# Optimization experiments

Hardware: AMD Instinct MI355X
Metric: run time of the kernel (lower is better)

## Reference

```python
import jax, jax.numpy as jnp
import numpy as np

LEVELS, REGIONS, Z_SIZE = 4, 8, 16
PHI_SIZE, OUT_SIZE, HIDDEN = 64, 32, 64
BATCH = 256
IN_SIZE = LEVELS * Z_SIZE + PHI_SIZE  # 128


def setup_inputs() -> dict:
    key = jax.random.key(0)
    ks = jax.random.split(key, 8)
    return {
        "phi": jax.random.normal(ks[0], (BATCH, PHI_SIZE), dtype=jnp.float32),
        "region_params": jax.random.normal(ks[1], (LEVELS, REGIONS, Z_SIZE), dtype=jnp.float32),
        "w1": jax.random.normal(ks[2], (HIDDEN, IN_SIZE), dtype=jnp.float32) * (1.0 / np.sqrt(IN_SIZE)),
        "b1": jax.random.normal(ks[3], (HIDDEN,), dtype=jnp.float32) * 0.01,
        "w2": jax.random.normal(ks[4], (HIDDEN, HIDDEN), dtype=jnp.float32) * (1.0 / np.sqrt(HIDDEN)),
        "b2": jax.random.normal(ks[5], (HIDDEN,), dtype=jnp.float32) * 0.01,
        "w3": jax.random.normal(ks[6], (OUT_SIZE, HIDDEN), dtype=jnp.float32) * (1.0 / np.sqrt(HIDDEN)),
        "b3": jax.random.normal(ks[7], (OUT_SIZE,), dtype=jnp.float32) * 0.01,
    }


def reference(phi, region_params, w1, b1, w2, b2, w3, b3):
    levels, regions, z_size = region_params.shape
    phi = phi.reshape(phi.shape[0], -1)
    batch, dim = phi.shape
    # Combinatorial grid of region choices per level (same as source: mgrid + .T indexing)
    i = jnp.mgrid[(slice(0, regions, 1),) * levels]  # (levels, regions, ..., regions)
    V_alphas = region_params[jnp.arange(levels), i.T].reshape(-1, levels * z_size)  # (R^L, latent_dim)
    n_combo = V_alphas.shape[0]
    phi_b = jnp.broadcast_to(phi[:, None, :], (batch, n_combo, dim))
    V_b = jnp.broadcast_to(V_alphas[None], (batch, n_combo, levels * z_size))
    X = jnp.concatenate([V_b, phi_b], axis=-1)  # (batch, R^L, in_size)
    # MLP: Linear->relu->Linear->relu->Linear
    h = jax.nn.relu(jnp.einsum("bci,hi->bch", X, w1) + b1)
    h = jax.nn.relu(jnp.einsum("bch,gh->bcg", h, w2) + b2)
    qs = jnp.einsum("bcg,og->bco", h, w3) + b3  # (batch, R^L, out_size)
    return qs
```

## Files before the change

kernel.cpp:

```cpp
#include <hip/hip_runtime.h>
#include <hip/hip_bf16.h>


typedef __attribute__((ext_vector_type(8))) short bf16x8;
typedef __attribute__((ext_vector_type(4))) short bf16x4;
typedef __attribute__((ext_vector_type(4))) float f32x4;

#define MFMA_K32(a, b, c) __builtin_amdgcn_mfma_f32_16x16x32_bf16(a, b, c, 0, 0, 0)

#if defined(__has_builtin)
#if __has_builtin(__builtin_amdgcn_mfma_f32_16x16x16bf16_1k)
#define MFMA_K16(a, b, c) __builtin_amdgcn_mfma_f32_16x16x16bf16_1k(a, b, c, 0, 0, 0)
#elif __has_builtin(__builtin_amdgcn_mfma_f32_16x16x16_bf16)
#define MFMA_K16(a, b, c) __builtin_amdgcn_mfma_f32_16x16x16_bf16(a, b, c, 0, 0, 0)
#endif
#endif
#ifndef MFMA_K16
__device__ __forceinline__ f32x4 mfma_k16_asm(bf16x4 a, bf16x4 b, f32x4 c) {
    f32x4 d;
    asm("v_mfma_f32_16x16x16_bf16 %0, %1, %2, %3" : "=v"(d) : "v"(a), "v"(b), "v"(c));
    return d;
}
#define MFMA_K16(a, b, c) mfma_k16_asm(a, b, c)
#endif

__device__ __forceinline__ short f2bf(float x) {
    union { __hip_bfloat16 b; short s; } u;
    u.b = __float2bfloat16(x);
    return u.s;
}

__device__ __forceinline__ float4 ldg4(const float* p) {
    return *reinterpret_cast<const float4*>(p);
}

__global__ __launch_bounds__(256, 4)
void zdec_kernel(const float* __restrict__ phi, const float* __restrict__ rp,
                 const float* __restrict__ w1, const float* __restrict__ b1,
                 const float* __restrict__ w2, const float* __restrict__ b2,
                 const float* __restrict__ w3, const float* __restrict__ b3,
                 float* __restrict__ out)
{
    __shared__ float smem[8256];
    float* const A01 = smem;
    float* const Bt  = smem + 4096;
    float* const Pt  = smem + 6144;
    float* const Ot  = smem + 6208;

    const int t   = threadIdx.x;
    const int b   = blockIdx.x >> 2;
    const int cbi = blockIdx.x & 3;

    {
        const int l = t >> 6, h = t & 63;
        float ws[16];
#pragma unroll
        for (int z4 = 0; z4 < 4; ++z4) {
            const float4 v = ldg4(w1 + h * 128 + l * 16 + z4 * 4);
            ws[z4*4+0] = v.x; ws[z4*4+1] = v.y; ws[z4*4+2] = v.z; ws[z4*4+3] = v.w;
        }
#pragma unroll
        for (int r = 0; r < 8; ++r) {
            float acc = 0.f;
#pragma unroll
            for (int z4 = 0; z4 < 4; ++z4) {
                const float4 v = ldg4(rp + (l * 8 + r) * 16 + z4 * 4);
                acc += ws[z4*4+0]*v.x + ws[z4*4+1]*v.y + ws[z4*4+2]*v.z + ws[z4*4+3]*v.w;
            }
            Bt[(l * 8 + r) * 64 + h] = acc;
        }
    }
    if (t < 64) {
        const int h = t;
        float acc = b1[h];
#pragma unroll
        for (int p4 = 0; p4 < 16; ++p4) {
            const float4 wv = ldg4(w1 + h * 128 + 64 + p4 * 4);
            const float4 pv = ldg4(phi + b * 64 + p4 * 4);
            acc += wv.x * pv.x + wv.y * pv.y + wv.z * pv.z + wv.w * pv.w;
        }
        Pt[h] = acc;
    }
    __syncthreads();
    {
        const int h = t & 63, cg = t >> 6;
#pragma unroll
        for (int cc2 = 0; cc2 < 16; ++cc2) {
            const int cc = cg * 16 + cc2;
            A01[cc * 64 + (h ^ ((cc & 15) << 2))] =
                Bt[(cc & 7) * 64 + h] + Bt[(8 + ((cc >> 3) & 7)) * 64 + h];
        }
    }
    __syncthreads();

    const int lane = t & 63;
    const int wid  = t >> 6;
    const int q = lane >> 4;
    const int s = lane & 15;
    const int row = (wid << 4) + s;
    const int amask = s << 2;

    bf16x8 w2f[4][2];
#pragma unroll
    for (int nt = 0; nt < 4; ++nt)
#pragma unroll
        for (int kt = 0; kt < 2; ++kt) {
            const float* src = w2 + (nt * 16 + s) * 64 + kt * 32 + q * 8;
            const float4 v0 = ldg4(src), v1 = ldg4(src + 4);
            bf16x8 f;
            f[0]=f2bf(v0.x); f[1]=f2bf(v0.y); f[2]=f2bf(v0.z); f[3]=f2bf(v0.w);
            f[4]=f2bf(v1.x); f[5]=f2bf(v1.y); f[6]=f2bf(v1.z); f[7]=f2bf(v1.w);
            w2f[nt][kt] = f;
        }
    bf16x4 w3f[2][4];
#pragma unroll
    for (int nt3 = 0; nt3 < 2; ++nt3)
#pragma unroll
        for (int nt = 0; nt < 4; ++nt) {
            const float4 v = ldg4(w3 + (nt3 * 16 + s) * 64 + nt * 16 + q * 4);
            bf16x4 f;
            f[0]=f2bf(v.x); f[1]=f2bf(v.y); f[2]=f2bf(v.z); f[3]=f2bf(v.w);
            w3f[nt3][nt] = f;
        }
    f32x4 b2i[4];
#pragma unroll
    for (int nt = 0; nt < 4; ++nt) {
        const float4 v = ldg4(b2 + nt * 16 + q * 4);
        b2i[nt] = f32x4{v.x, v.y, v.z, v.w};
    }
    f32x4 b3i[2];
#pragma unroll
    for (int nt3 = 0; nt3 < 2; ++nt3) {
        const float4 v = ldg4(b3 + nt3 * 16 + q * 4);
        b3i[nt3] = f32x4{v.x, v.y, v.z, v.w};
    }

    float* const ot = Ot + (wid << 9);
    float* const gwbase = out + ((size_t)b * 4096 + (cbi << 10) + (wid << 4)) * 32;

    for (int mhi = 0; mhi < 2; ++mhi) {
        const float* bt3 = Bt + (24 + (((cbi << 1) + mhi) & 7)) * 64;
        float ap3[16];
#pragma unroll
        for (int c4 = 0; c4 < 4; ++c4) {
            const int hc = (c4 >> 1) * 32 + q * 8 + (c4 & 1) * 4;
            const f32x4 av = *reinterpret_cast<const f32x4*>(A01 + row * 64 + (hc ^ amask));
            const f32x4 pv = *reinterpret_cast<const f32x4*>(Pt + hc);
            const f32x4 v3 = *reinterpret_cast<const f32x4*>(bt3 + hc);
#pragma unroll
            for (int j = 0; j < 4; ++j) ap3[c4*4+j] = av[j] + pv[j] + v3[j];
        }
#pragma unroll
        for (int mlo = 0; mlo < 8; ++mlo) {
            const float* bt2 = Bt + (16 + mlo) * 64;
            bf16x8 h1f0, h1f1;
            {
                float tmp[16];
#pragma unroll
                for (int c4 = 0; c4 < 4; ++c4) {
                    const int hc = (c4 >> 1) * 32 + q * 8 + (c4 & 1) * 4;
                    const f32x4 v2 = *reinterpret_cast<const f32x4*>(bt2 + hc);
#pragma unroll
                    for (int j = 0; j < 4; ++j)
                        tmp[c4*4+j] = fmaxf(ap3[c4*4+j] + v2[j], 0.f);
                }
#pragma unroll
                for (int j = 0; j < 8; ++j) h1f0[j] = f2bf(tmp[j]);
#pragma unroll
                for (int j = 0; j < 8; ++j) h1f1[j] = f2bf(tmp[8 + j]);
            }
            f32x4 a2[4];
#pragma unroll
            for (int nt = 0; nt < 4; ++nt) {
                f32x4 acc = b2i[nt];
                acc = MFMA_K32(w2f[nt][0], h1f0, acc);
                acc = MFMA_K32(w2f[nt][1], h1f1, acc);
                a2[nt] = acc;
            }
            bf16x4 h2f[4];
#pragma unroll
            for (int nt = 0; nt < 4; ++nt) {
                bf16x4 f;
#pragma unroll
                for (int r = 0; r < 4; ++r) f[r] = f2bf(fmaxf(a2[nt][r], 0.f));
                h2f[nt] = f;
            }
#pragma unroll
            for (int nt3 = 0; nt3 < 2; ++nt3) {
                f32x4 acc = b3i[nt3];
#pragma unroll
                for (int nt = 0; nt < 4; ++nt)
                    acc = MFMA_K16(w3f[nt3][nt], h2f[nt], acc);
                const int c = (nt3 * 4 + q) ^ (s & 7);
                *reinterpret_cast<f32x4*>(ot + s * 32 + c * 4) = acc;
            }
            asm volatile("s_waitcnt lgkmcnt(0)" ::: "memory");
            {
                float* gb = gwbase + (mhi * 8 + mlo) * 2048;
#pragma unroll
                for (int k = 0; k < 2; ++k) {
                    const int sr = k * 8 + (lane >> 3);
                    const int cr = (lane & 7) ^ (sr & 7);
                    const f32x4 v = *reinterpret_cast<const f32x4*>(ot + sr * 32 + cr * 4);
                    *reinterpret_cast<f32x4*>(gb + k * 256 + lane * 4) = v;
                }
            }
        }
    }
}

extern "C" void kernel_launch(void* const* d_in, const int* in_sizes, int n_in,
                              void* d_out, int out_size, void* d_ws, size_t ws_size,
                              hipStream_t stream) {
    const float* phi = (const float*)d_in[0];
    const float* rp  = (const float*)d_in[1];
    const float* w1  = (const float*)d_in[2];
    const float* b1  = (const float*)d_in[3];
    const float* w2  = (const float*)d_in[4];
    const float* b2  = (const float*)d_in[5];
    const float* w3  = (const float*)d_in[6];
    const float* b3  = (const float*)d_in[7];
    (void)in_sizes; (void)n_in; (void)out_size; (void)d_ws; (void)ws_size;

    zdec_kernel<<<dim3(1024), dim3(256), 0, stream>>>(
        phi, rp, w1, b1, w2, b2, w3, b3, (float*)d_out);
}
```

Measured before the change: 42.28 us.

## Drop A01 LDS staging, keep layer-1 sums in registers, defer output stores

Removes the shared-memory A01 table and its extra barrier. Each thread now builds its two level-0/1/3 plus phi partial sums directly in registers from Bt. The loop order is swapped so the level-2 row is loaded once per mlo. Each tile's global store is deferred until the next tile's compute and the explicit lgkmcnt wait is dropped, so LDS readback and global writes overlap with MFMA work. LDS use roughly halves, which may allow more resident blocks, at the cost of extra registers for the two partial-sum arrays.

```diff
diff --git a/kernel.cpp b/kernel.cpp
--- a/kernel.cpp
+++ b/kernel.cpp
@@ -41,11 +41,10 @@
                  const float* __restrict__ w3, const float* __restrict__ b3,
                  float* __restrict__ out)
 {
-    __shared__ float smem[8256];
-    float* const A01 = smem;
-    float* const Bt  = smem + 4096;
-    float* const Pt  = smem + 6144;
-    float* const Ot  = smem + 6208;
+    __shared__ float smem[4160];
+    float* const Bt = smem;
+    float* const Pt = smem + 2048;
+    float* const Ot = smem + 2112;
 
     const int t   = threadIdx.x;
     const int b   = blockIdx.x >> 2;
@@ -80,16 +79,6 @@
             acc += wv.x * pv.x + wv.y * pv.y + wv.z * pv.z + wv.w * pv.w;
         }
         Pt[h] = acc;
-    }
-    __syncthreads();
-    {
-        const int h = t & 63, cg = t >> 6;
-#pragma unroll
-        for (int cc2 = 0; cc2 < 16; ++cc2) {
-            const int cc = cg * 16 + cc2;
-            A01[cc * 64 + (h ^ ((cc & 15) << 2))] =
-                Bt[(cc & 7) * 64 + h] + Bt[(8 + ((cc >> 3) & 7)) * 64 + h];
-        }
     }
     __syncthreads();
 
@@ -98,7 +87,6 @@
     const int q = lane >> 4;
     const int s = lane & 15;
     const int row = (wid << 4) + s;
-    const int amask = s << 2;
 
     bf16x8 w2f[4][2];
 #pragma unroll
@@ -135,35 +123,65 @@
         b3i[nt3] = f32x4{v.x, v.y, v.z, v.w};
     }
 
+    float afp[2][16];
+    {
+        const float* a0  = Bt + ((row & 7)) * 64;
+        const float* a1  = Bt + (8 + ((row >> 3) & 7)) * 64;
+        const float* t3a = Bt + (24 + 2 * cbi) * 64;
+        const float* t3b = Bt + (24 + 2 * cbi + 1) * 64;
+#pragma unroll
+        for (int c4 = 0; c4 < 4; ++c4) {
+            const int hc = (c4 >> 1) * 32 + q * 8 + (c4 & 1) * 4;
+            const f32x4 v0 = *reinterpret_cast<const f32x4*>(a0 + hc);
+            const f32x4 v1 = *reinterpret_cast<const f32x4*>(a1 + hc);
+            const f32x4 vp = *reinterpret_cast<const f32x4*>(Pt + hc);
+            const f32x4 w0 = *reinterpret_cast<const f32x4*>(t3a + hc);
+            const f32x4 w1v = *reinterpret_cast<const f32x4*>(t3b + hc);
+#pragma unroll
+            for (int j = 0; j < 4; ++j) {
+                const float base = v0[j] + v1[j] + vp[j];
+                afp[0][c4*4+j] = base + w0[j];
+                afp[1][c4*4+j] = base + w1v[j];
+            }
+        }
+    }
+
     float* const ot = Ot + (wid << 9);
     float* const gwbase = out + ((size_t)b * 4096 + (cbi << 10) + (wid << 4)) * 32;
 
-    for (int mhi = 0; mhi < 2; ++mhi) {
-        const float* bt3 = Bt + (24 + (((cbi << 1) + mhi) & 7)) * 64;
-        float ap3[16];
-#pragma unroll
-        for (int c4 = 0; c4 < 4; ++c4) {
-            const int hc = (c4 >> 1) * 32 + q * 8 + (c4 & 1) * 4;
-            const f32x4 av = *reinterpret_cast<const f32x4*>(A01 + row * 64 + (hc ^ amask));
-            const f32x4 pv = *reinterpret_cast<const f32x4*>(Pt + hc);
-            const f32x4 v3 = *reinterpret_cast<const f32x4*>(bt3 + hc);
-#pragma unroll
-            for (int j = 0; j < 4; ++j) ap3[c4*4+j] = av[j] + pv[j] + v3[j];
-        }
-#pragma unroll
-        for (int mlo = 0; mlo < 8; ++mlo) {
+#pragma unroll
+    for (int mlo = 0; mlo < 8; ++mlo) {
+        float b2r[16];
+        {
             const float* bt2 = Bt + (16 + mlo) * 64;
+#pragma unroll
+            for (int c4 = 0; c4 < 4; ++c4) {
+                const int hc = (c4 >> 1) * 32 + q * 8 + (c4 & 1) * 4;
+                const f32x4 v = *reinterpret_cast<const f32x4*>(bt2 + hc);
+#pragma unroll
+                for (int j = 0; j < 4; ++j) b2r[c4*4+j] = v[j];
+            }
+        }
+#pragma unroll
+        for (int mhi = 0; mhi < 2; ++mhi) {
+            const int k = mlo * 2 + mhi;
+            if (k > 0) {
+                const int mtp = ((k - 1) & 1) * 8 + ((k - 1) >> 1);
+                float* gb = gwbase + mtp * 2048;
+#pragma unroll
+                for (int kk = 0; kk < 2; ++kk) {
+                    const int sr = kk * 8 + (lane >> 3);
+                    const int cr = (lane & 7) ^ (sr & 7);
+                    const f32x4 v = *reinterpret_cast<const f32x4*>(ot + sr * 32 + cr * 4);
+                    *reinterpret_cast<f32x4*>(gb + kk * 256 + lane * 4) = v;
+                }
+            }
             bf16x8 h1f0, h1f1;
             {
                 float tmp[16];
 #pragma unroll
-                for (int c4 = 0; c4 < 4; ++c4) {
-                    const int hc = (c4 >> 1) * 32 + q * 8 + (c4 & 1) * 4;
-                    const f32x4 v2 = *reinterpret_cast<const f32x4*>(bt2 + hc);
-#pragma unroll
-                    for (int j = 0; j < 4; ++j)
-                        tmp[c4*4+j] = fmaxf(ap3[c4*4+j] + v2[j], 0.f);
-                }
+                for (int j = 0; j < 16; ++j)
+                    tmp[j] = fmaxf(afp[mhi][j] + b2r[j], 0.f);
 #pragma unroll
                 for (int j = 0; j < 8; ++j) h1f0[j] = f2bf(tmp[j]);
 #pragma unroll
@@ -194,17 +212,16 @@
                 const int c = (nt3 * 4 + q) ^ (s & 7);
                 *reinterpret_cast<f32x4*>(ot + s * 32 + c * 4) = acc;
             }
-            asm volatile("s_waitcnt lgkmcnt(0)" ::: "memory");
-            {
-                float* gb = gwbase + (mhi * 8 + mlo) * 2048;
-#pragma unroll
-                for (int k = 0; k < 2; ++k) {
-                    const int sr = k * 8 + (lane >> 3);
-                    const int cr = (lane & 7) ^ (sr & 7);
-                    const f32x4 v = *reinterpret_cast<const f32x4*>(ot + sr * 32 + cr * 4);
-                    *reinterpret_cast<f32x4*>(gb + k * 256 + lane * 4) = v;
-                }
-            }
+        }
+    }
+    {
+        float* gb = gwbase + 15 * 2048;
+#pragma unroll
+        for (int kk = 0; kk < 2; ++kk) {
+            const int sr = kk * 8 + (lane >> 3);
+            const int cr = (lane & 7) ^ (sr & 7);
+            const f32x4 v = *reinterpret_cast<const f32x4*>(ot + sr * 32 + cr * 4);
+            *reinterpret_cast<f32x4*>(gb + kk * 256 + lane * 4) = v;
         }
     }
 }
```

New measurement: 109.0 us. +157.7%, slower.
